# Kernel optimization log

Measured on AMD Instinct MI355X. Metric: run time of the kernel, lower is better.

The kernel has to match this reference:

```python
import jax, jax.numpy as jnp
import numpy as np
import math

B, L, D = 8, 2048, 256


def setup_inputs() -> dict:
    key = jax.random.key(0)
    ks = jax.random.split(key, 8)
    return {
        "query": jax.random.normal(ks[0], (B, L, D), dtype=jnp.float32),
        "key": jax.random.normal(ks[1], (B, L, D), dtype=jnp.float32),
        "value": jax.random.normal(ks[2], (B, L, D), dtype=jnp.float32),
        "mask": jax.random.randint(ks[3], (B, L), 0, 2, dtype=jnp.int32),
        "Wq_w": jax.random.normal(ks[4], (D, D), dtype=jnp.float32) * 0.05,
        "Wq_b": jax.random.normal(ks[5], (D,), dtype=jnp.float32) * 0.05,
        "Wk_w": jax.random.normal(ks[6], (D, D), dtype=jnp.float32) * 0.05,
        "Wk_b": jax.random.normal(ks[7], (D,), dtype=jnp.float32) * 0.05,
    }


def reference(query, key, value, mask, Wq_w, Wq_b, Wk_w, Wk_b):
    d = query.shape[-1]
    q = query @ Wq_w.T + Wq_b            # [B, Lq, D]
    k = key @ Wk_w.T + Wk_b              # [B, Lk, D]
    scores = jnp.einsum("bqd,bkd->bqk", q, k) / math.sqrt(d)  # [B, Lq, Lk]
    m = mask.astype(scores.dtype)[:, None, :]                  # [B, 1, Lk]
    # multiplicative then additive masking, as in original
    scores = jnp.where(m == 0, jnp.asarray(-1e9, scores.dtype), scores * m)
    attn = jax.nn.softmax(scores, axis=-1)
    return jnp.einsum("bqk,bkd->bqd", attn, value)
```

## Files before the change

kernel.cpp:

```cpp
#include <hip/hip_runtime.h>
#include <stdint.h>
#include <stddef.h>

#define B_ 8
#define L_ 2048
#define D_ 256
#define KSPLIT 4
#define KRANGE 512
#define KTILE 32
#define NITER 16

typedef __bf16 bf16x8 __attribute__((ext_vector_type(8)));
typedef float floatx4 __attribute__((ext_vector_type(4)));
typedef float floatx16 __attribute__((ext_vector_type(16)));
typedef _Float16 half4_t __attribute__((ext_vector_type(4)));

__device__ __forceinline__ short f2bf(float f) {
    union { float f; uint32_t u; } v; v.f = f;
    return (short)((v.u + 0x8000u) >> 16);
}

__device__ __forceinline__ uint32_t pack2bf(float a, float b) {
    union { float f; uint32_t u; } x, y; x.f = a; y.f = b;
    return ((x.u + 0x8000u) >> 16) | ((y.u + 0x8000u) & 0xFFFF0000u);
}

__device__ __forceinline__ uint32_t cvtpk_bf16(float lo, float hi2) {
    uint32_t w;
    asm("v_cvt_pk_bf16_f32 %0, %1, %2" : "=v"(w) : "v"(lo), "v"(hi2));
    return w;
}

__device__ __forceinline__ void pl32swap(uint32_t &a, uint32_t &b) {
    asm("v_permlane32_swap_b32 %0, %1" : "+v"(a), "+v"(b));
}

__device__ __forceinline__ void async16(const void* g, void* l) {
    __builtin_amdgcn_global_load_lds(
        (__attribute__((address_space(1))) void*)g,
        (__attribute__((address_space(3))) void*)l,
        16, 0, 0);
}

__global__ __launch_bounds__(256, 3) void proj_kernel(
    const float* __restrict__ Xq, const float* __restrict__ Xk,
    const float* __restrict__ Wq, const float* __restrict__ Wk,
    const float* __restrict__ bq, const float* __restrict__ bk,
    short* __restrict__ Oq, short* __restrict__ Ok)
{
    const float* X    = blockIdx.y ? Xk : Xq;
    const float* W    = blockIdx.y ? Wk : Wq;
    const float* bias = blockIdx.y ? bk : bq;
    short* Out        = blockIdx.y ? Ok : Oq;

    __shared__ uint32_t As[2][64 * 20];
    __shared__ uint32_t Ws[2][256 * 20];

    const int tid  = threadIdx.x;
    const int wid  = tid >> 6;
    const int lane = tid & 63;
    const int m16  = lane & 15;
    const int quad = lane >> 4;
    const int row0 = blockIdx.x * 64;
    const int ar = tid >> 2, cg = tid & 3;

    floatx4 acc[16];
    const floatx4 z4 = {0.f, 0.f, 0.f, 0.f};
#pragma unroll
    for (int i = 0; i < 16; i++) acc[i] = z4;

    {
        const float* srcA = X + (size_t)(row0 + ar) * D_ + cg * 8;
        float4 a = *(const float4*)srcA, b2 = *(const float4*)(srcA + 4);
        uint4 u; u.x = pack2bf(a.x, a.y); u.y = pack2bf(a.z, a.w);
        u.z = pack2bf(b2.x, b2.y); u.w = pack2bf(b2.z, b2.w);
        *(uint4*)&As[0][ar * 20 + cg * 4] = u;
#pragma unroll
        for (int p = 0; p < 4; p++) {
            const float* srcW = W + (size_t)(p * 64 + ar) * D_ + cg * 8;
            float4 wa = *(const float4*)srcW, wb = *(const float4*)(srcW + 4);
            uint4 w; w.x = pack2bf(wa.x, wa.y); w.y = pack2bf(wa.z, wa.w);
            w.z = pack2bf(wb.x, wb.y); w.w = pack2bf(wb.z, wb.w);
            *(uint4*)&Ws[0][(p * 64 + ar) * 20 + cg * 4] = w;
        }
    }
    __syncthreads();

    for (int kc = 0; kc < 8; kc++) {
        const int buf = kc & 1;
        float4 na, nb, nwa[4], nwb[4];
        if (kc < 7) {
            const int k1 = (kc + 1) * 32;
            const float* srcA = X + (size_t)(row0 + ar) * D_ + k1 + cg * 8;
            na = *(const float4*)srcA; nb = *(const float4*)(srcA + 4);
#pragma unroll
            for (int p = 0; p < 4; p++) {
                const float* srcW = W + (size_t)(p * 64 + ar) * D_ + k1 + cg * 8;
                nwa[p] = *(const float4*)srcW; nwb[p] = *(const float4*)(srcW + 4);
            }
        }
        bf16x8 af = *(const bf16x8*)&As[buf][(wid * 16 + m16) * 20 + quad * 4];
#pragma unroll
        for (int n = 0; n < 16; n++) {
            bf16x8 bfr = *(const bf16x8*)&Ws[buf][(n * 16 + m16) * 20 + quad * 4];
            acc[n] = __builtin_amdgcn_mfma_f32_16x16x32_bf16(af, bfr, acc[n], 0, 0, 0);
        }
        if (kc < 7) {
            uint4 u; u.x = pack2bf(na.x, na.y); u.y = pack2bf(na.z, na.w);
            u.z = pack2bf(nb.x, nb.y); u.w = pack2bf(nb.z, nb.w);
            *(uint4*)&As[buf ^ 1][ar * 20 + cg * 4] = u;
#pragma unroll
            for (int p = 0; p < 4; p++) {
                uint4 w; w.x = pack2bf(nwa[p].x, nwa[p].y); w.y = pack2bf(nwa[p].z, nwa[p].w);
                w.z = pack2bf(nwb[p].x, nwb[p].y); w.w = pack2bf(nwb[p].z, nwb[p].w);
                *(uint4*)&Ws[buf ^ 1][(p * 64 + ar) * 20 + cg * 4] = w;
            }
        }
        __syncthreads();
    }
#pragma unroll
    for (int n = 0; n < 16; n++) {
        const int col = n * 16 + m16;
        const float bv = bias[col];
#pragma unroll
        for (int r = 0; r < 4; r++) {
            const int row = row0 + wid * 16 + quad * 4 + r;
            Out[(size_t)row * D_ + col] = f2bf(acc[n][r] + bv);
        }
    }
}

__global__ __launch_bounds__(256, 2) void vtrans_kernel(
    const float* __restrict__ V, short* __restrict__ Vt)
{
    __shared__ uint32_t T[256 * 20];
    const int tid = threadIdx.x;
    const int b  = blockIdx.y;
    const int l0 = blockIdx.x * 32;
    const int r2 = tid >> 4;
    const int dg = tid & 15;
    const int lp = r2 ^ ((dg & 3) << 2);
#pragma unroll
    for (int p = 0; p < 4; p++) {
        int d0 = (dg + p * 16) * 4;
        const float* src = V + ((size_t)b * L_ + l0 + r2 * 2) * D_ + d0;
        float4 e0 = *(const float4*)src;
        float4 e1 = *(const float4*)(src + D_);
        T[(d0 + 0) * 20 + lp] = pack2bf(e0.x, e1.x);
        T[(d0 + 1) * 20 + lp] = pack2bf(e0.y, e1.y);
        T[(d0 + 2) * 20 + lp] = pack2bf(e0.z, e1.z);
        T[(d0 + 3) * 20 + lp] = pack2bf(e0.w, e1.w);
    }
    __syncthreads();
#pragma unroll
    for (int p = 0; p < 4; p++) {
        int d = (tid >> 2) + p * 64;
        int c = tid & 3;
        int cp = c ^ ((d >> 2) & 3);
        uint4 u = *(const uint4*)&T[d * 20 + cp * 4];
        *(uint4*)(Vt + ((size_t)b * D_ + d) * L_ + l0 + c * 8) = u;
    }
}

__global__ __launch_bounds__(512, 2) void flash_kernel(
    const short* __restrict__ Qb, const short* __restrict__ Kb,
    const short* __restrict__ Vt, const int* __restrict__ mask,
    float* __restrict__ Out, _Float16* __restrict__ Part,
    float* __restrict__ Lpart)
{
    __shared__ short Ks[2][KTILE * 256];
    __shared__ short Vs[2][256 * KTILE];

    const int tid  = threadIdx.x;
    const int wid  = tid >> 6;
    const int lane = tid & 63;
    const int l31  = lane & 31;
    const int hi   = lane >> 5;
    const int b  = blockIdx.x;
    const int q0 = blockIdx.y * 256;
    const int z  = blockIdx.z;

    const char* kgb = (const char*)(Kb + ((size_t)b * L_ + z * KRANGE) * D_);
    const char* vgb = (const char*)(Vt + (size_t)b * D_ * L_ + z * KRANGE);
    const int*  mg  = mask + b * L_ + z * KRANGE;

    bf16x8 qf[16];
    {
        const short* qrow = Qb + ((size_t)b * L_ + q0 + wid * 32 + l31) * D_ + hi * 8;
#pragma unroll
        for (int dt = 0; dt < 16; dt++)
            qf[dt] = *(const bf16x8*)(qrow + dt * 16);
    }

    uint32_t mbits = 0;
#pragma unroll
    for (int t = 0; t < NITER; t++)
        mbits |= (mg[t * KTILE + l31] != 0 ? 1u : 0u) << t;

    floatx16 o[8];
#pragma unroll
    for (int n = 0; n < 8; n++)
#pragma unroll
        for (int r = 0; r < 16; r++) o[n][r] = 0.f;
    float rsum = 0.f;

    const int KBb = l31 * 512 + ((((l31 & 7) ^ ((l31 >> 3) & 3)) ^ hi) << 4);
    const int VBb = l31 * 64 + (((((l31 >> 1) & 3) ^ ((l31 >> 3) & 1)) ^ hi) << 4);

    int koff[2], voff[2];
#pragma unroll
    for (int c = 0; c < 2; c++) {
        int row = wid * 4 + c * 2 + hi;
        int gk = l31 ^ (row & 7) ^ ((row >> 3) & 3);
        koff[c] = row * 512 + gk * 16;
        int d = (wid * 2 + c) * 16 + (lane >> 2);
        int gv = (lane & 3) ^ ((lane >> 3) & 3) ^ ((lane >> 5) & 1);
        voff[c] = d * (L_ * 2) + gv * 16;
    }

#pragma unroll
    for (int c = 0; c < 2; c++)
        async16(kgb + koff[c], &Ks[0][0] + (wid * 2 + c) * 512);
#pragma unroll
    for (int c = 0; c < 2; c++)
        async16(vgb + voff[c], &Vs[1][0] + (wid * 2 + c) * 512);
    __builtin_amdgcn_s_waitcnt(0x0F70);
    __syncthreads();

    const float C2 = 0.09016844f;
    bf16x8 pfA, pfB;
    {
        union { uint32_t u[4]; bf16x8 v; } zz;
        zz.u[0] = 0; zz.u[1] = 0; zz.u[2] = 0; zz.u[3] = 0;
        pfA = zz.v; pfB = zz.v;
    }

    for (int t2 = 0; t2 < NITER; t2 += 2) {
#pragma unroll
        for (int half = 0; half < 2; half++) {
            const int t = t2 + half;
            const int buf = half;

            {
                const char* kp = kgb + (size_t)((t + 1) & 15) * (KTILE * D_ * 2);
                const char* vp = vgb + (size_t)t * (KTILE * 2);
#pragma unroll
                for (int c = 0; c < 2; c++)
                    async16(kp + koff[c], &Ks[buf ^ 1][0] + (wid * 2 + c) * 512);
#pragma unroll
                for (int c = 0; c < 2; c++)
                    async16(vp + voff[c], &Vs[buf][0] + (wid * 2 + c) * 512);
            }

            const char* kl = (const char*)&Ks[buf][0];
            floatx16 s0, s1;
#pragma unroll
            for (int r = 0; r < 16; r++) { s0[r] = 0.f; s1[r] = 0.f; }
            __builtin_amdgcn_s_setprio(1);
#pragma unroll
            for (int dt = 0; dt < 16; dt += 2) {
                bf16x8 kf0 = *(const bf16x8*)(kl + (KBb ^ (dt << 5)));
                bf16x8 kf1 = *(const bf16x8*)(kl + (KBb ^ ((dt + 1) << 5)));
                s0 = __builtin_amdgcn_mfma_f32_32x32x16_bf16(kf0, qf[dt], s0, 0, 0, 0);
                s1 = __builtin_amdgcn_mfma_f32_32x32x16_bf16(kf1, qf[dt + 1], s1, 0, 0, 0);
            }

            const char* vl = (const char*)&Vs[buf ^ 1][0];
#pragma unroll
            for (int n = 0; n < 8; n++) {
                bf16x8 vf0 = *(const bf16x8*)(vl + (VBb ^ (n << 11)));
                bf16x8 vf1 = *(const bf16x8*)(vl + (VBb ^ ((n << 11) | 32)));
                o[n] = __builtin_amdgcn_mfma_f32_32x32x16_bf16(pfA, vf0, o[n], 0, 0, 0);
                o[n] = __builtin_amdgcn_mfma_f32_32x32x16_bf16(pfB, vf1, o[n], 0, 0, 0);
            }
            __builtin_amdgcn_s_setprio(0);

            uint32_t mb = (uint32_t)__ballot((mbits >> t) & 1) >> (hi * 4);
            uint32_t w[8];
#pragma unroll
            for (int i = 0; i < 8; i++) {
                const int r0 = 2 * i, r1 = 2 * i + 1;
                const int k0 = (r0 & 3) + 8 * (r0 >> 2);
                float sv0 = s0[r0] + s1[r0];
                float sv1 = s0[r1] + s1[r1];
                float e0 = ((mb >> k0) & 1) ? exp2f(sv0 * C2) : 0.f;
                float e1 = ((mb >> (k0 + 1)) & 1) ? exp2f(sv1 * C2) : 0.f;
                rsum += e0 + e1;
                w[i] = cvtpk_bf16(e0, e1);
            }
            pl32swap(w[0], w[2]); pl32swap(w[1], w[3]);
            pl32swap(w[4], w[6]); pl32swap(w[5], w[7]);
            {
                union { uint32_t u[4]; bf16x8 v; } ua, ub;
                ua.u[0] = w[0]; ua.u[1] = w[1]; ua.u[2] = w[2]; ua.u[3] = w[3];
                ub.u[0] = w[4]; ub.u[1] = w[5]; ub.u[2] = w[6]; ub.u[3] = w[7];
                pfA = ua.v; pfB = ub.v;
            }

            __syncthreads();
        }
    }

    {
        const char* vl = (const char*)&Vs[1][0];
        __builtin_amdgcn_s_setprio(1);
#pragma unroll
        for (int n = 0; n < 8; n++) {
            bf16x8 vf0 = *(const bf16x8*)(vl + (VBb ^ (n << 11)));
            bf16x8 vf1 = *(const bf16x8*)(vl + (VBb ^ ((n << 11) | 32)));
            o[n] = __builtin_amdgcn_mfma_f32_32x32x16_bf16(pfA, vf0, o[n], 0, 0, 0);
            o[n] = __builtin_amdgcn_mfma_f32_32x32x16_bf16(pfB, vf1, o[n], 0, 0, 0);
        }
        __builtin_amdgcn_s_setprio(0);
    }

    rsum += __shfl_xor(rsum, 32);

    const size_t BLD = (size_t)B_ * L_ * D_;
    const size_t rowbase = (size_t)b * L_ + q0 + wid * 32;
    if (z == 0) {
        float* po = Out + rowbase * D_;
#pragma unroll
        for (int n = 0; n < 8; n++)
#pragma unroll
            for (int r = 0; r < 16; r++) {
                int q = (r & 3) + 8 * (r >> 2) + 4 * hi;
                po[(size_t)q * D_ + n * 32 + l31] = o[n][r];
            }
    } else {
        _Float16* pp = Part + (size_t)(z - 1) * BLD + rowbase * D_;
#pragma unroll
        for (int n = 0; n < 8; n++)
#pragma unroll
            for (int r = 0; r < 16; r++) {
                int q = (r & 3) + 8 * (r >> 2) + 4 * hi;
                pp[(size_t)q * D_ + n * 32 + l31] = (_Float16)o[n][r];
            }
    }
    if (lane < 32) {
        Lpart[(size_t)z * (B_ * L_) + rowbase + lane] = rsum;
    }
}

__global__ __launch_bounds__(256) void norm_kernel(
    float* __restrict__ Out, const _Float16* __restrict__ Part,
    const float* __restrict__ Lpart)
{
    const int idx = blockIdx.x * 256 + threadIdx.x;
    const int row = idx >> 6;
    const int c   = (idx & 63) * 4;
    const size_t off = (size_t)row * D_ + c;
    const size_t BLD = (size_t)B_ * L_ * D_;
    float4 acc = *(float4*)(Out + off);
#pragma unroll
    for (int zz = 0; zz < 3; zz++) {
        half4_t h = *(const half4_t*)(Part + zz * BLD + off);
        acc.x += (float)h.x; acc.y += (float)h.y;
        acc.z += (float)h.z; acc.w += (float)h.w;
    }
    const int BL = B_ * L_;
    float l = Lpart[row] + Lpart[BL + row] + Lpart[2 * BL + row] + Lpart[3 * BL + row];
    float inv = 1.0f / l;
    acc.x *= inv; acc.y *= inv; acc.z *= inv; acc.w *= inv;
    *(float4*)(Out + off) = acc;
}

extern "C" void kernel_launch(void* const* d_in, const int* in_sizes, int n_in,
                              void* d_out, int out_size, void* d_ws, size_t ws_size,
                              hipStream_t stream) {
    const float* query = (const float*)d_in[0];
    const float* key   = (const float*)d_in[1];
    const float* value = (const float*)d_in[2];
    const int*   mask  = (const int*)d_in[3];
    const float* Wq_w  = (const float*)d_in[4];
    const float* Wq_b  = (const float*)d_in[5];
    const float* Wk_w  = (const float*)d_in[6];
    const float* Wk_b  = (const float*)d_in[7];
    float* out = (float*)d_out;

    const size_t BLD = (size_t)B_ * L_ * D_;
    short* qb = (short*)d_ws;
    short* kb = qb + BLD;
    short* vt = kb + BLD;
    _Float16* part = (_Float16*)(vt + BLD);
    float* lpart = (float*)(part + 3 * BLD);

    proj_kernel<<<dim3(256, 2), 256, 0, stream>>>(query, key, Wq_w, Wk_w, Wq_b, Wk_b, qb, kb);
    vtrans_kernel<<<dim3(64, 8), 256, 0, stream>>>(value, vt);
    flash_kernel<<<dim3(8, 8, 4), 512, 0, stream>>>(qb, kb, vt, mask, out, part, lpart);
    norm_kernel<<<dim3((B_ * L_ * D_ / 4) / 256), 256, 0, stream>>>(out, part, lpart);
}
```

Measured before the change: 178.2 us.

## Double key tile to 64 per iteration, halving barriers and pipelining PV with softmax

Raises the key tile from 32 to 64 rows so each loop iteration handles two 32-key sub-tiles. This halves the number of __syncthreads barriers and async-load rounds. Within an iteration, the QK MFMA chain for each sub-tile is now interleaved with the PV MFMAs of the previous tile and its softmax, and the split s0/s1 accumulators are replaced by a single chain. LDS use doubles (K tile 32KB per buffer) and more register state is live (four P fragments), which could reduce occupancy below the launch-bounds target or cause spills.

```diff
diff --git a/kernel.cpp b/kernel.cpp
--- a/kernel.cpp
+++ b/kernel.cpp
@@ -5,10 +5,9 @@
 #define B_ 8
 #define L_ 2048
 #define D_ 256
-#define KSPLIT 4
 #define KRANGE 512
-#define KTILE 32
-#define NITER 16
+#define KTILE 64
+#define NITER 8
 
 typedef __bf16 bf16x8 __attribute__((ext_vector_type(8)));
 typedef float floatx4 __attribute__((ext_vector_type(4)));
@@ -169,7 +168,7 @@
     float* __restrict__ Lpart)
 {
     __shared__ short Ks[2][KTILE * 256];
-    __shared__ short Vs[2][256 * KTILE];
+    __shared__ short Vs[4][256 * 32];
 
     const int tid  = threadIdx.x;
     const int wid  = tid >> 6;
@@ -195,7 +194,7 @@
     uint32_t mbits = 0;
 #pragma unroll
     for (int t = 0; t < NITER; t++)
-        mbits |= (mg[t * KTILE + l31] != 0 ? 1u : 0u) << t;
+        mbits |= (mg[t * KTILE + lane] != 0 ? 1u : 0u) << t;
 
     floatx16 o[8];
 #pragma unroll
@@ -207,33 +206,67 @@
     const int KBb = l31 * 512 + ((((l31 & 7) ^ ((l31 >> 3) & 3)) ^ hi) << 4);
     const int VBb = l31 * 64 + (((((l31 >> 1) & 3) ^ ((l31 >> 3) & 1)) ^ hi) << 4);
 
-    int koff[2], voff[2];
-#pragma unroll
-    for (int c = 0; c < 2; c++) {
-        int row = wid * 4 + c * 2 + hi;
+    int koff[4], voff[2];
+#pragma unroll
+    for (int c = 0; c < 4; c++) {
+        int row = wid * 8 + c * 2 + hi;
         int gk = l31 ^ (row & 7) ^ ((row >> 3) & 3);
         koff[c] = row * 512 + gk * 16;
+    }
+#pragma unroll
+    for (int c = 0; c < 2; c++) {
         int d = (wid * 2 + c) * 16 + (lane >> 2);
         int gv = (lane & 3) ^ ((lane >> 3) & 3) ^ ((lane >> 5) & 1);
         voff[c] = d * (L_ * 2) + gv * 16;
     }
 
 #pragma unroll
-    for (int c = 0; c < 2; c++)
-        async16(kgb + koff[c], &Ks[0][0] + (wid * 2 + c) * 512);
-#pragma unroll
-    for (int c = 0; c < 2; c++)
-        async16(vgb + voff[c], &Vs[1][0] + (wid * 2 + c) * 512);
+    for (int c = 0; c < 4; c++)
+        async16(kgb + koff[c], &Ks[0][0] + (wid * 4 + c) * 512);
+#pragma unroll
+    for (int c = 0; c < 2; c++) {
+        async16(vgb + voff[c],      &Vs[2][0] + (wid * 2 + c) * 512);
+        async16(vgb + 64 + voff[c], &Vs[3][0] + (wid * 2 + c) * 512);
+    }
     __builtin_amdgcn_s_waitcnt(0x0F70);
     __syncthreads();
 
     const float C2 = 0.09016844f;
-    bf16x8 pfA, pfB;
+    bf16x8 pfA, pfB, pfC, pfD;
     {
         union { uint32_t u[4]; bf16x8 v; } zz;
         zz.u[0] = 0; zz.u[1] = 0; zz.u[2] = 0; zz.u[3] = 0;
-        pfA = zz.v; pfB = zz.v;
-    }
+        pfA = zz.v; pfB = zz.v; pfC = zz.v; pfD = zz.v;
+    }
+
+    auto softmax32 = [&](const floatx16& s, uint32_t mb, bf16x8& pA, bf16x8& pB) {
+        uint32_t w[8];
+#pragma unroll
+        for (int i = 0; i < 8; i++) {
+            const int r0 = 2 * i, r1 = 2 * i + 1;
+            const int k0 = (r0 & 3) + 8 * (r0 >> 2);
+            float e0 = ((mb >> k0) & 1) ? exp2f(s[r0] * C2) : 0.f;
+            float e1 = ((mb >> (k0 + 1)) & 1) ? exp2f(s[r1] * C2) : 0.f;
+            rsum += e0 + e1;
+            w[i] = cvtpk_bf16(e0, e1);
+        }
+        pl32swap(w[0], w[2]); pl32swap(w[1], w[3]);
+        pl32swap(w[4], w[6]); pl32swap(w[5], w[7]);
+        union { uint32_t u[4]; bf16x8 v; } ua, ub;
+        ua.u[0] = w[0]; ua.u[1] = w[1]; ua.u[2] = w[2]; ua.u[3] = w[3];
+        ub.u[0] = w[4]; ub.u[1] = w[5]; ub.u[2] = w[6]; ub.u[3] = w[7];
+        pA = ua.v; pB = ub.v;
+    };
+
+    auto pvhalf = [&](const char* vl, bf16x8 pA, bf16x8 pB) {
+#pragma unroll
+        for (int n = 0; n < 8; n++) {
+            bf16x8 vf0 = *(const bf16x8*)(vl + (VBb ^ (n << 11)));
+            bf16x8 vf1 = *(const bf16x8*)(vl + (VBb ^ ((n << 11) | 32)));
+            o[n] = __builtin_amdgcn_mfma_f32_32x32x16_bf16(pA, vf0, o[n], 0, 0, 0);
+            o[n] = __builtin_amdgcn_mfma_f32_32x32x16_bf16(pB, vf1, o[n], 0, 0, 0);
+        }
+    };
 
     for (int t2 = 0; t2 < NITER; t2 += 2) {
 #pragma unroll
@@ -242,77 +275,60 @@
             const int buf = half;
 
             {
-                const char* kp = kgb + (size_t)((t + 1) & 15) * (KTILE * D_ * 2);
+                const char* kp = kgb + (size_t)((t + 1) & (NITER - 1)) * (KTILE * D_ * 2);
                 const char* vp = vgb + (size_t)t * (KTILE * 2);
 #pragma unroll
-                for (int c = 0; c < 2; c++)
-                    async16(kp + koff[c], &Ks[buf ^ 1][0] + (wid * 2 + c) * 512);
-#pragma unroll
-                for (int c = 0; c < 2; c++)
-                    async16(vp + voff[c], &Vs[buf][0] + (wid * 2 + c) * 512);
-            }
-
-            const char* kl = (const char*)&Ks[buf][0];
-            floatx16 s0, s1;
-#pragma unroll
-            for (int r = 0; r < 16; r++) { s0[r] = 0.f; s1[r] = 0.f; }
+                for (int c = 0; c < 4; c++)
+                    async16(kp + koff[c], &Ks[buf ^ 1][0] + (wid * 4 + c) * 512);
+#pragma unroll
+                for (int c = 0; c < 2; c++) {
+                    async16(vp + voff[c],      &Vs[buf * 2][0]     + (wid * 2 + c) * 512);
+                    async16(vp + 64 + voff[c], &Vs[buf * 2 + 1][0] + (wid * 2 + c) * 512);
+                }
+            }
+
+            const char* kl  = (const char*)&Ks[buf][0];
+            const char* vl0 = (const char*)&Vs[(buf ^ 1) * 2][0];
+            const char* vl1 = (const char*)&Vs[(buf ^ 1) * 2 + 1][0];
+            uint64_t bal = __ballot((mbits >> t) & 1);
+
             __builtin_amdgcn_s_setprio(1);
-#pragma unroll
-            for (int dt = 0; dt < 16; dt += 2) {
-                bf16x8 kf0 = *(const bf16x8*)(kl + (KBb ^ (dt << 5)));
-                bf16x8 kf1 = *(const bf16x8*)(kl + (KBb ^ ((dt + 1) << 5)));
-                s0 = __builtin_amdgcn_mfma_f32_32x32x16_bf16(kf0, qf[dt], s0, 0, 0, 0);
-                s1 = __builtin_amdgcn_mfma_f32_32x32x16_bf16(kf1, qf[dt + 1], s1, 0, 0, 0);
-            }
-
-            const char* vl = (const char*)&Vs[buf ^ 1][0];
-#pragma unroll
-            for (int n = 0; n < 8; n++) {
-                bf16x8 vf0 = *(const bf16x8*)(vl + (VBb ^ (n << 11)));
-                bf16x8 vf1 = *(const bf16x8*)(vl + (VBb ^ ((n << 11) | 32)));
-                o[n] = __builtin_amdgcn_mfma_f32_32x32x16_bf16(pfA, vf0, o[n], 0, 0, 0);
-                o[n] = __builtin_amdgcn_mfma_f32_32x32x16_bf16(pfB, vf1, o[n], 0, 0, 0);
-            }
+
+            floatx16 s;
+#pragma unroll
+            for (int r = 0; r < 16; r++) s[r] = 0.f;
+#pragma unroll
+            for (int dt = 0; dt < 16; dt++) {
+                bf16x8 kf = *(const bf16x8*)(kl + (KBb ^ (dt << 5)));
+                s = __builtin_amdgcn_mfma_f32_32x32x16_bf16(kf, qf[dt], s, 0, 0, 0);
+            }
+
+            pvhalf(vl0, pfA, pfB);
+
+            softmax32(s, (uint32_t)bal >> (hi * 4), pfA, pfB);
+
+#pragma unroll
+            for (int r = 0; r < 16; r++) s[r] = 0.f;
+#pragma unroll
+            for (int dt = 0; dt < 16; dt++) {
+                bf16x8 kf = *(const bf16x8*)(kl + 16384 + (KBb ^ (dt << 5)));
+                s = __builtin_amdgcn_mfma_f32_32x32x16_bf16(kf, qf[dt], s, 0, 0, 0);
+            }
+
+            pvhalf(vl1, pfC, pfD);
+
+            softmax32(s, (uint32_t)(bal >> 32) >> (hi * 4), pfC, pfD);
+
             __builtin_amdgcn_s_setprio(0);
 
-            uint32_t mb = (uint32_t)__ballot((mbits >> t) & 1) >> (hi * 4);
-            uint32_t w[8];
-#pragma unroll
-            for (int i = 0; i < 8; i++) {
-                const int r0 = 2 * i, r1 = 2 * i + 1;
-                const int k0 = (r0 & 3) + 8 * (r0 >> 2);
-                float sv0 = s0[r0] + s1[r0];
-                float sv1 = s0[r1] + s1[r1];
-                float e0 = ((mb >> k0) & 1) ? exp2f(sv0 * C2) : 0.f;
-                float e1 = ((mb >> (k0 + 1)) & 1) ? exp2f(sv1 * C2) : 0.f;
-                rsum += e0 + e1;
-                w[i] = cvtpk_bf16(e0, e1);
-            }
-            pl32swap(w[0], w[2]); pl32swap(w[1], w[3]);
-            pl32swap(w[4], w[6]); pl32swap(w[5], w[7]);
-            {
-                union { uint32_t u[4]; bf16x8 v; } ua, ub;
-                ua.u[0] = w[0]; ua.u[1] = w[1]; ua.u[2] = w[2]; ua.u[3] = w[3];
-                ub.u[0] = w[4]; ub.u[1] = w[5]; ub.u[2] = w[6]; ub.u[3] = w[7];
-                pfA = ua.v; pfB = ub.v;
-            }
-
             __syncthreads();
         }
     }
 
-    {
-        const char* vl = (const char*)&Vs[1][0];
-        __builtin_amdgcn_s_setprio(1);
-#pragma unroll
-        for (int n = 0; n < 8; n++) {
-            bf16x8 vf0 = *(const bf16x8*)(vl + (VBb ^ (n << 11)));
-            bf16x8 vf1 = *(const bf16x8*)(vl + (VBb ^ ((n << 11) | 32)));
-            o[n] = __builtin_amdgcn_mfma_f32_32x32x16_bf16(pfA, vf0, o[n], 0, 0, 0);
-            o[n] = __builtin_amdgcn_mfma_f32_32x32x16_bf16(pfB, vf1, o[n], 0, 0, 0);
-        }
-        __builtin_amdgcn_s_setprio(0);
-    }
+    __builtin_amdgcn_s_setprio(1);
+    pvhalf((const char*)&Vs[2][0], pfA, pfB);
+    pvhalf((const char*)&Vs[3][0], pfC, pfD);
+    __builtin_amdgcn_s_setprio(0);
 
     rsum += __shfl_xor(rsum, 32);
 
```

After: 183.7 us. 1.03x slower.

## Triple-buffer K/V tiles with partial vmcnt wait and fragment-native partial layout

Applied to the files above, without the earlier changes.

Moves the flash kernel's K/V shared-memory staging from double to triple buffering. Loads are now issued two tiles ahead, and the barrier waits with vmcnt(4), so the newest prefetch can stay in flight across the sync. The fp16 partial outputs are also written in the MFMA fragment order as contiguous 16-byte vectors, and the norm kernel reads them back in that order. This trades coalesced partial writes and reads for scattered fp32 accesses to Out in the norm kernel, and shared memory use grows by half, which may lower occupancy.

```diff
diff --git a/kernel.cpp b/kernel.cpp
--- a/kernel.cpp
+++ b/kernel.cpp
@@ -5,7 +5,6 @@
 #define B_ 8
 #define L_ 2048
 #define D_ 256
-#define KSPLIT 4
 #define KRANGE 512
 #define KTILE 32
 #define NITER 16
@@ -14,6 +13,7 @@
 typedef float floatx4 __attribute__((ext_vector_type(4)));
 typedef float floatx16 __attribute__((ext_vector_type(16)));
 typedef _Float16 half4_t __attribute__((ext_vector_type(4)));
+typedef _Float16 half8_t __attribute__((ext_vector_type(8)));
 
 __device__ __forceinline__ short f2bf(float f) {
     union { float f; uint32_t u; } v; v.f = f;
@@ -168,8 +168,8 @@
     float* __restrict__ Out, _Float16* __restrict__ Part,
     float* __restrict__ Lpart)
 {
-    __shared__ short Ks[2][KTILE * 256];
-    __shared__ short Vs[2][256 * KTILE];
+    __shared__ short Ks[3][KTILE * 256];
+    __shared__ short Vs[3][256 * KTILE];
 
     const int tid  = threadIdx.x;
     const int wid  = tid >> 6;
@@ -177,7 +177,8 @@
     const int l31  = lane & 31;
     const int hi   = lane >> 5;
     const int b  = blockIdx.x;
-    const int q0 = blockIdx.y * 256;
+    const int yb = blockIdx.y;
+    const int q0 = yb * 256;
     const int z  = blockIdx.z;
 
     const char* kgb = (const char*)(Kb + ((size_t)b * L_ + z * KRANGE) * D_);
@@ -219,11 +220,12 @@
     }
 
 #pragma unroll
-    for (int c = 0; c < 2; c++)
-        async16(kgb + koff[c], &Ks[0][0] + (wid * 2 + c) * 512);
-#pragma unroll
-    for (int c = 0; c < 2; c++)
-        async16(vgb + voff[c], &Vs[1][0] + (wid * 2 + c) * 512);
+    for (int c = 0; c < 2; c++) {
+        async16(kgb + koff[c], (char*)&Ks[0][0] + (wid * 2 + c) * 1024);
+        async16(vgb + voff[c], (char*)&Vs[2][0] + (wid * 2 + c) * 1024);
+        async16(kgb + (KTILE * D_ * 2) + koff[c], (char*)&Ks[1][0] + (wid * 2 + c) * 1024);
+        async16(vgb + voff[c], (char*)&Vs[0][0] + (wid * 2 + c) * 1024);
+    }
     __builtin_amdgcn_s_waitcnt(0x0F70);
     __syncthreads();
 
@@ -235,75 +237,34 @@
         pfA = zz.v; pfB = zz.v;
     }
 
-    for (int t2 = 0; t2 < NITER; t2 += 2) {
-#pragma unroll
-        for (int half = 0; half < 2; half++) {
-            const int t = t2 + half;
-            const int buf = half;
-
-            {
-                const char* kp = kgb + (size_t)((t + 1) & 15) * (KTILE * D_ * 2);
-                const char* vp = vgb + (size_t)t * (KTILE * 2);
-#pragma unroll
-                for (int c = 0; c < 2; c++)
-                    async16(kp + koff[c], &Ks[buf ^ 1][0] + (wid * 2 + c) * 512);
-#pragma unroll
-                for (int c = 0; c < 2; c++)
-                    async16(vp + voff[c], &Vs[buf][0] + (wid * 2 + c) * 512);
+    short* kCur = &Ks[0][0]; short* kNxt = &Ks[1][0]; short* kDst = &Ks[2][0];
+    short* vP   = &Vs[2][0]; short* vQ   = &Vs[0][0]; short* vR   = &Vs[1][0];
+
+    for (int t = 0; t < NITER; t++) {
+        {
+            const char* kp = kgb + (size_t)((t + 2) & 15) * (KTILE * D_ * 2);
+            const char* vp = vgb + (size_t)((t + 1) & 15) * (KTILE * 2);
+#pragma unroll
+            for (int c = 0; c < 2; c++) {
+                async16(kp + koff[c], (char*)kDst + (wid * 2 + c) * 1024);
+                async16(vp + voff[c], (char*)vR + (wid * 2 + c) * 1024);
             }
-
-            const char* kl = (const char*)&Ks[buf][0];
-            floatx16 s0, s1;
-#pragma unroll
-            for (int r = 0; r < 16; r++) { s0[r] = 0.f; s1[r] = 0.f; }
-            __builtin_amdgcn_s_setprio(1);
-#pragma unroll
-            for (int dt = 0; dt < 16; dt += 2) {
-                bf16x8 kf0 = *(const bf16x8*)(kl + (KBb ^ (dt << 5)));
-                bf16x8 kf1 = *(const bf16x8*)(kl + (KBb ^ ((dt + 1) << 5)));
-                s0 = __builtin_amdgcn_mfma_f32_32x32x16_bf16(kf0, qf[dt], s0, 0, 0, 0);
-                s1 = __builtin_amdgcn_mfma_f32_32x32x16_bf16(kf1, qf[dt + 1], s1, 0, 0, 0);
-            }
-
-            const char* vl = (const char*)&Vs[buf ^ 1][0];
-#pragma unroll
-            for (int n = 0; n < 8; n++) {
-                bf16x8 vf0 = *(const bf16x8*)(vl + (VBb ^ (n << 11)));
-                bf16x8 vf1 = *(const bf16x8*)(vl + (VBb ^ ((n << 11) | 32)));
-                o[n] = __builtin_amdgcn_mfma_f32_32x32x16_bf16(pfA, vf0, o[n], 0, 0, 0);
-                o[n] = __builtin_amdgcn_mfma_f32_32x32x16_bf16(pfB, vf1, o[n], 0, 0, 0);
-            }
-            __builtin_amdgcn_s_setprio(0);
-
-            uint32_t mb = (uint32_t)__ballot((mbits >> t) & 1) >> (hi * 4);
-            uint32_t w[8];
-#pragma unroll
-            for (int i = 0; i < 8; i++) {
-                const int r0 = 2 * i, r1 = 2 * i + 1;
-                const int k0 = (r0 & 3) + 8 * (r0 >> 2);
-                float sv0 = s0[r0] + s1[r0];
-                float sv1 = s0[r1] + s1[r1];
-                float e0 = ((mb >> k0) & 1) ? exp2f(sv0 * C2) : 0.f;
-                float e1 = ((mb >> (k0 + 1)) & 1) ? exp2f(sv1 * C2) : 0.f;
-                rsum += e0 + e1;
-                w[i] = cvtpk_bf16(e0, e1);
-            }
-            pl32swap(w[0], w[2]); pl32swap(w[1], w[3]);
-            pl32swap(w[4], w[6]); pl32swap(w[5], w[7]);
-            {
-                union { uint32_t u[4]; bf16x8 v; } ua, ub;
-                ua.u[0] = w[0]; ua.u[1] = w[1]; ua.u[2] = w[2]; ua.u[3] = w[3];
-                ub.u[0] = w[4]; ub.u[1] = w[5]; ub.u[2] = w[6]; ub.u[3] = w[7];
-                pfA = ua.v; pfB = ub.v;
-            }
-
-            __syncthreads();
-        }
-    }
-
-    {
-        const char* vl = (const char*)&Vs[1][0];
+        }
+
+        const char* kl = (const char*)kCur;
+        floatx16 s0, s1;
+#pragma unroll
+        for (int r = 0; r < 16; r++) { s0[r] = 0.f; s1[r] = 0.f; }
         __builtin_amdgcn_s_setprio(1);
+#pragma unroll
+        for (int dt = 0; dt < 16; dt += 2) {
+            bf16x8 kf0 = *(const bf16x8*)(kl + (KBb ^ (dt << 5)));
+            bf16x8 kf1 = *(const bf16x8*)(kl + (KBb ^ ((dt + 1) << 5)));
+            s0 = __builtin_amdgcn_mfma_f32_32x32x16_bf16(kf0, qf[dt], s0, 0, 0, 0);
+            s1 = __builtin_amdgcn_mfma_f32_32x32x16_bf16(kf1, qf[dt + 1], s1, 0, 0, 0);
+        }
+
+        const char* vl = (const char*)vP;
 #pragma unroll
         for (int n = 0; n < 8; n++) {
             bf16x8 vf0 = *(const bf16x8*)(vl + (VBb ^ (n << 11)));
@@ -312,6 +273,48 @@
             o[n] = __builtin_amdgcn_mfma_f32_32x32x16_bf16(pfB, vf1, o[n], 0, 0, 0);
         }
         __builtin_amdgcn_s_setprio(0);
+
+        uint32_t mb = (uint32_t)__ballot((mbits >> t) & 1) >> (hi * 4);
+        uint32_t w[8];
+#pragma unroll
+        for (int i = 0; i < 8; i++) {
+            const int r0 = 2 * i, r1 = 2 * i + 1;
+            const int k0 = (r0 & 3) + 8 * (r0 >> 2);
+            float sv0 = s0[r0] + s1[r0];
+            float sv1 = s0[r1] + s1[r1];
+            float e0 = ((mb >> k0) & 1) ? exp2f(sv0 * C2) : 0.f;
+            float e1 = ((mb >> (k0 + 1)) & 1) ? exp2f(sv1 * C2) : 0.f;
+            rsum += e0 + e1;
+            w[i] = cvtpk_bf16(e0, e1);
+        }
+        pl32swap(w[0], w[2]); pl32swap(w[1], w[3]);
+        pl32swap(w[4], w[6]); pl32swap(w[5], w[7]);
+        {
+            union { uint32_t u[4]; bf16x8 v; } ua, ub;
+            ua.u[0] = w[0]; ua.u[1] = w[1]; ua.u[2] = w[2]; ua.u[3] = w[3];
+            ub.u[0] = w[4]; ub.u[1] = w[5]; ub.u[2] = w[6]; ub.u[3] = w[7];
+            pfA = ua.v; pfB = ub.v;
+        }
+
+        asm volatile("s_waitcnt vmcnt(4)" ::: "memory");
+        __builtin_amdgcn_s_barrier();
+        asm volatile("" ::: "memory");
+
+        short* tk = kCur; kCur = kNxt; kNxt = kDst; kDst = tk;
+        short* tv = vP;   vP = vQ;     vQ = vR;     vR = tv;
+    }
+
+    {
+        const char* vl = (const char*)vP;
+        __builtin_amdgcn_s_setprio(1);
+#pragma unroll
+        for (int n = 0; n < 8; n++) {
+            bf16x8 vf0 = *(const bf16x8*)(vl + (VBb ^ (n << 11)));
+            bf16x8 vf1 = *(const bf16x8*)(vl + (VBb ^ ((n << 11) | 32)));
+            o[n] = __builtin_amdgcn_mfma_f32_32x32x16_bf16(pfA, vf0, o[n], 0, 0, 0);
+            o[n] = __builtin_amdgcn_mfma_f32_32x32x16_bf16(pfB, vf1, o[n], 0, 0, 0);
+        }
+        __builtin_amdgcn_s_setprio(0);
     }
 
     rsum += __shfl_xor(rsum, 32);
@@ -328,13 +331,16 @@
                 po[(size_t)q * D_ + n * 32 + l31] = o[n][r];
             }
     } else {
-        _Float16* pp = Part + (size_t)(z - 1) * BLD + rowbase * D_;
+        _Float16* pp = Part + (size_t)(z - 1) * BLD;
 #pragma unroll
         for (int n = 0; n < 8; n++)
 #pragma unroll
-            for (int r = 0; r < 16; r++) {
-                int q = (r & 3) + 8 * (r >> 2) + 4 * hi;
-                pp[(size_t)q * D_ + n * 32 + l31] = (_Float16)o[n][r];
+            for (int h2 = 0; h2 < 2; h2++) {
+                half8_t hv;
+#pragma unroll
+                for (int i = 0; i < 8; i++) hv[i] = (_Float16)o[n][h2 * 8 + i];
+                size_t cidx = ((((size_t)((b * 8 + yb) * 8 + wid)) * 8 + n) * 2 + h2) * 64 + lane;
+                *(half8_t*)(pp + cidx * 8) = hv;
             }
     }
     if (lane < 32) {
@@ -346,23 +352,37 @@
     float* __restrict__ Out, const _Float16* __restrict__ Part,
     const float* __restrict__ Lpart)
 {
-    const int idx = blockIdx.x * 256 + threadIdx.x;
-    const int row = idx >> 6;
-    const int c   = (idx & 63) * 4;
-    const size_t off = (size_t)row * D_ + c;
+    const int gid  = blockIdx.x * 256 + threadIdx.x;
+    const int lane = gid & 63;
+    const int h2   = (gid >> 6) & 1;
+    const int n    = (gid >> 7) & 7;
+    const int w    = (gid >> 10) & 7;
+    const int yb   = (gid >> 13) & 7;
+    const int b    = gid >> 16;
+    const int l31  = lane & 31, hi = lane >> 5;
+    const int d    = n * 32 + l31;
+    const int rowbase = b * L_ + yb * 256 + w * 32;
     const size_t BLD = (size_t)B_ * L_ * D_;
-    float4 acc = *(float4*)(Out + off);
+    const int BL = B_ * L_;
+
+    float acc[8];
+#pragma unroll
+    for (int i = 0; i < 8; i++) acc[i] = 0.f;
 #pragma unroll
     for (int zz = 0; zz < 3; zz++) {
-        half4_t h = *(const half4_t*)(Part + zz * BLD + off);
-        acc.x += (float)h.x; acc.y += (float)h.y;
-        acc.z += (float)h.z; acc.w += (float)h.w;
-    }
-    const int BL = B_ * L_;
-    float l = Lpart[row] + Lpart[BL + row] + Lpart[2 * BL + row] + Lpart[3 * BL + row];
-    float inv = 1.0f / l;
-    acc.x *= inv; acc.y *= inv; acc.z *= inv; acc.w *= inv;
-    *(float4*)(Out + off) = acc;
+        half8_t hv = *(const half8_t*)(Part + zz * BLD + (size_t)gid * 8);
+#pragma unroll
+        for (int i = 0; i < 8; i++) acc[i] += (float)hv[i];
+    }
+#pragma unroll
+    for (int i = 0; i < 8; i++) {
+        const int r = h2 * 8 + i;
+        const int q = (r & 3) + 8 * (r >> 2) + 4 * hi;
+        const int row = rowbase + q;
+        float l = Lpart[row] + Lpart[BL + row] + Lpart[2 * BL + row] + Lpart[3 * BL + row];
+        const size_t off = (size_t)row * D_ + d;
+        Out[off] = (Out[off] + acc[i]) / l;
+    }
 }
 
 extern "C" void kernel_launch(void* const* d_in, const int* in_sizes, int n_in,
@@ -388,5 +408,5 @@
     proj_kernel<<<dim3(256, 2), 256, 0, stream>>>(query, key, Wq_w, Wk_w, Wq_b, Wk_b, qb, kb);
     vtrans_kernel<<<dim3(64, 8), 256, 0, stream>>>(value, vt);
     flash_kernel<<<dim3(8, 8, 4), 512, 0, stream>>>(qb, kb, vt, mask, out, part, lpart);
-    norm_kernel<<<dim3((B_ * L_ * D_ / 4) / 256), 256, 0, stream>>>(out, part, lpart);
-}
+    norm_kernel<<<dim3((B_ * L_ * D_ / 8) / 256), 256, 0, stream>>>(out, part, lpart);
+}
```

Measured after the change: 167.8 us. 5.8% less time.
